# Kernel optimization log

Measured on AMD Instinct MI355X. Metric: run time of the kernel, lower is better.

The kernel has to match this reference:

```python
import jax, jax.numpy as jnp
import numpy as np

N_NODES = 100000
IN_CH = 128
HIDDEN = 256
N_EDGES = 500000


def setup_inputs() -> dict:
    key = jax.random.key(0)
    k1, k2, k3, k4, k5, k6 = jax.random.split(key, 6)
    latent_space = jax.random.normal(k1, (N_NODES, IN_CH), dtype=jnp.float32)
    edge_index = jax.random.randint(k2, (2, N_EDGES), 0, N_NODES, dtype=jnp.int64)
    # torch Linear params: W is [out, in], y = x @ W.T + b
    lim1 = 1.0 / np.sqrt(2 * IN_CH)
    W1 = jax.random.uniform(k3, (HIDDEN, 2 * IN_CH), minval=-lim1, maxval=lim1, dtype=jnp.float32)
    b1 = jax.random.uniform(k4, (HIDDEN,), minval=-lim1, maxval=lim1, dtype=jnp.float32)
    lim2 = 1.0 / np.sqrt(HIDDEN)
    W2 = jax.random.uniform(k5, (1, HIDDEN), minval=-lim2, maxval=lim2, dtype=jnp.float32)
    b2 = jax.random.uniform(k6, (1,), minval=-lim2, maxval=lim2, dtype=jnp.float32)
    return {"latent_space": latent_space, "W1": W1, "b1": b1, "W2": W2, "b2": b2,
            "edge_index": edge_index}


def reference(latent_space, W1, b1, W2, b2, edge_index):
    src, dst = edge_index[0], edge_index[1]
    h_src = latent_space[src]                      # [E, C]
    h_dst = latent_space[dst]                      # [E, C]
    h_pair = jnp.concatenate([h_src, h_dst], axis=1)  # [E, 2C]
    h = jax.nn.relu(h_pair @ W1.T + b1)            # [E, H]; dropout=0 (eval)
    logits = (h @ W2.T + b2).squeeze(-1)           # [E]
    return jax.nn.sigmoid(logits)
```

## Files before the change

### kernel.cpp

```cpp
#include <hip/hip_runtime.h>
#include <hip/hip_bf16.h>
#include <stdint.h>

#define M_NODES 100000
#define E_EDGES 500000
#define NCOL    512
#define HID     256

typedef unsigned short u16;
typedef u16   u16x8 __attribute__((ext_vector_type(8)));
typedef u16   u16x4 __attribute__((ext_vector_type(4)));
typedef __bf16 bf16x8 __attribute__((ext_vector_type(8)));
typedef float f32x4 __attribute__((ext_vector_type(4)));

static __device__ __forceinline__ u16 f2bf(float f) {
  uint32_t u = __float_as_uint(f);
  u += 0x7fff + ((u >> 16) & 1);
  return (u16)(u >> 16);
}
static __device__ __forceinline__ float bf2f(u16 h) {
  return __uint_as_float(((uint32_t)h) << 16);
}

__global__ __launch_bounds__(256) void k_convert(const float* __restrict__ in,
                                                 u16* __restrict__ out, int n4) {
  int i = blockIdx.x * blockDim.x + threadIdx.x;
  int stride = gridDim.x * blockDim.x;
  for (; i < n4; i += stride) {
    float4 f = reinterpret_cast<const float4*>(in)[i];
    u16x4 o;
    o[0] = f2bf(f.x); o[1] = f2bf(f.y); o[2] = f2bf(f.z); o[3] = f2bf(f.w);
    reinterpret_cast<u16x4*>(out)[i] = o;
  }
}

__global__ __launch_bounds__(256) void k_weights(const float* __restrict__ W1,
                                                 u16* __restrict__ Bt) {
  int idx = blockIdx.x * 256 + threadIdx.x;
  int j = idx >> 7, k = idx & 127;
  float w = (j < HID) ? W1[j * 256 + k] : W1[(j - HID) * 256 + 128 + k];
  Bt[idx] = f2bf(w);
}

__global__ __launch_bounds__(256, 2) void k_gemm(const u16* __restrict__ A,
                                                 const u16* __restrict__ Bt,
                                                 const float* __restrict__ b1,
                                                 u16* __restrict__ UV) {
  __shared__ __align__(16) u16 ldsA[128 * 128];
  __shared__ __align__(16) u16 ldsB[128 * 128];
  const int t = threadIdx.x;
  const int bm = blockIdx.x, bn = blockIdx.y;

  {
    const int sub = t >> 4;
    const int slot = t & 15;
    #pragma unroll
    for (int r = 0; r < 8; ++r) {
      int row = r * 16 + sub;
      int sw = (slot ^ (row & 7)) * 8;
      int grow = bm * 128 + row; if (grow > M_NODES - 1) grow = M_NODES - 1;
      u16x8 va = *reinterpret_cast<const u16x8*>(A + (size_t)grow * 128 + slot * 8);
      *reinterpret_cast<u16x8*>(&ldsA[row * 128 + sw]) = va;
      int brow = bn * 128 + row;
      u16x8 vb = *reinterpret_cast<const u16x8*>(Bt + (size_t)brow * 128 + slot * 8);
      *reinterpret_cast<u16x8*>(&ldsB[row * 128 + sw]) = vb;
    }
  }
  __syncthreads();

  const int w  = t >> 6;
  const int l  = t & 63;
  const int wm = (w >> 1) * 64;
  const int wn = (w & 1) * 64;
  const int lr = l & 15;
  const int lk = l >> 4;

  f32x4 acc[4][4];
  #pragma unroll
  for (int i = 0; i < 4; ++i)
    #pragma unroll
    for (int j = 0; j < 4; ++j) acc[i][j] = f32x4{0.f, 0.f, 0.f, 0.f};

  #pragma unroll
  for (int kk = 0; kk < 128; kk += 32) {
    const int s = (kk >> 3) + lk;
    bf16x8 fa[4], fb[4];
    #pragma unroll
    for (int mt = 0; mt < 4; ++mt) {
      int row = wm + mt * 16 + lr;
      fa[mt] = *reinterpret_cast<const bf16x8*>(&ldsA[row * 128 + ((s ^ (row & 7)) * 8)]);
    }
    #pragma unroll
    for (int nt = 0; nt < 4; ++nt) {
      int row = wn + nt * 16 + lr;
      fb[nt] = *reinterpret_cast<const bf16x8*>(&ldsB[row * 128 + ((s ^ (row & 7)) * 8)]);
    }
    #pragma unroll
    for (int nt = 0; nt < 4; ++nt)
      #pragma unroll
      for (int mt = 0; mt < 4; ++mt)
        acc[nt][mt] = __builtin_amdgcn_mfma_f32_16x16x32_bf16(fb[nt], fa[mt], acc[nt][mt], 0, 0, 0);
  }

  #pragma unroll
  for (int nt = 0; nt < 4; ++nt) {
    #pragma unroll
    for (int mt = 0; mt < 4; ++mt) {
      int mg = bm * 128 + wm + mt * 16 + lr;
      int ng = bn * 128 + wn + nt * 16 + lk * 4;
      if (mg < M_NODES) {
        u16x4 o;
        #pragma unroll
        for (int r = 0; r < 4; ++r) {
          float v = acc[nt][mt][r];
          int col = ng + r;
          if (col < HID) v += b1[col];
          o[r] = f2bf(v);
        }
        *reinterpret_cast<u16x4*>(&UV[(size_t)mg * NCOL + ng]) = o;
      }
    }
  }
}

__global__ __launch_bounds__(256) void k_edge(const u16* __restrict__ UV,
                                              const int* __restrict__ src,
                                              const int* __restrict__ dst,
                                              const float* __restrict__ W2,
                                              const float* __restrict__ b2p,
                                              float* __restrict__ out) {
  const int t = threadIdx.x;
  const int hl = t & 31;
  const int hw = blockIdx.x * 8 + (t >> 5);
  const int nhw = gridDim.x * 8;

  float w2r[8];
  #pragma unroll
  for (int i = 0; i < 8; ++i) w2r[i] = W2[hl * 8 + i];
  const float b2 = *b2p;

  for (int e = hw; e < E_EDGES; e += nhw) {
    int s = src[e];
    int d = dst[e];
    u16x8 uu = *reinterpret_cast<const u16x8*>(UV + (size_t)s * NCOL + hl * 8);
    u16x8 vv = *reinterpret_cast<const u16x8*>(UV + (size_t)d * NCOL + HID + hl * 8);
    float a = 0.f;
    #pragma unroll
    for (int i = 0; i < 8; ++i) {
      float h = bf2f(uu[i]) + bf2f(vv[i]);
      h = fmaxf(h, 0.f);
      a = fmaf(h, w2r[i], a);
    }
    a += __shfl_xor(a, 16, 64);
    a += __shfl_xor(a, 8, 64);
    a += __shfl_xor(a, 4, 64);
    a += __shfl_xor(a, 2, 64);
    a += __shfl_xor(a, 1, 64);
    if (hl == 0) {
      out[e] = 1.0f / (1.0f + __expf(-(a + b2)));
    }
  }
}

extern "C" void kernel_launch(void* const* d_in, const int* in_sizes, int n_in,
                              void* d_out, int out_size, void* d_ws, size_t ws_size,
                              hipStream_t stream) {
  const float* latent = (const float*)d_in[0];
  const float* W1     = (const float*)d_in[1];
  const float* b1     = (const float*)d_in[2];
  const float* W2     = (const float*)d_in[3];
  const float* b2     = (const float*)d_in[4];
  const int*   eidx   = (const int*)d_in[5];

  char* ws = (char*)d_ws;
  u16* latent_bf = (u16*)ws;
  u16* Btw       = (u16*)(ws + 25600000);
  u16* UV        = (u16*)(ws + 25600000 + 131072);

  k_convert<<<2048, 256, 0, stream>>>(latent, latent_bf, (M_NODES * 128) / 4);
  k_weights<<<256, 256, 0, stream>>>(W1, Btw);
  dim3 gg((M_NODES + 127) / 128, NCOL / 128);
  k_gemm<<<gg, 256, 0, stream>>>(latent_bf, Btw, b1, UV);
  k_edge<<<1024, 256, 0, stream>>>(UV, eidx, eidx + E_EDGES, W2, b2, (float*)d_out);
}
```

Before: 236.3 us.

## Use direct global-to-LDS loads in GEMM and widen per-lane edge gathers

The GEMM tile load now uses global_load_lds to write A and pre-swizzled B straight into shared memory, bypassing registers. To make that work, the weight prep kernel now writes B already XOR-swizzled, and the A source address is permuted per lane. The edge kernel now handles four edges per wavefront with 16 lanes each, and each lane loads 32 bytes per side. It also gets a larger grid and an occupancy hint. This is meant to cut register staging in the GEMM and raise the number of gathers in flight in the edge pass, at the cost of more complex addressing.

```diff
diff --git a/kernel.cpp b/kernel.cpp
--- a/kernel.cpp
+++ b/kernel.cpp
@@ -21,6 +21,11 @@
 static __device__ __forceinline__ float bf2f(u16 h) {
   return __uint_as_float(((uint32_t)h) << 16);
 }
+
+#define GLOAD_LDS16(g, lds)                                                          \
+  __builtin_amdgcn_global_load_lds(                                                  \
+      (const __attribute__((address_space(1))) uint32_t*)(g),                        \
+      (__attribute__((address_space(3))) uint32_t*)(lds), 16, 0, 0)
 
 __global__ __launch_bounds__(256) void k_convert(const float* __restrict__ in,
                                                  u16* __restrict__ out, int n4) {
@@ -37,7 +42,10 @@
 __global__ __launch_bounds__(256) void k_weights(const float* __restrict__ W1,
                                                  u16* __restrict__ Bt) {
   int idx = blockIdx.x * 256 + threadIdx.x;
-  int j = idx >> 7, k = idx & 127;
+  int j = idx >> 7, kk = idx & 127;
+  int s = kk >> 3, i = kk & 7;
+  int ls = s ^ (j & 7);
+  int k = ls * 8 + i;
   float w = (j < HID) ? W1[j * 256 + k] : W1[(j - HID) * 256 + 128 + k];
   Bt[idx] = f2bf(w);
 }
@@ -50,26 +58,24 @@
   __shared__ __align__(16) u16 ldsB[128 * 128];
   const int t = threadIdx.x;
   const int bm = blockIdx.x, bn = blockIdx.y;
+  const int w = t >> 6, l = t & 63;
 
   {
-    const int sub = t >> 4;
-    const int slot = t & 15;
-    #pragma unroll
-    for (int r = 0; r < 8; ++r) {
-      int row = r * 16 + sub;
-      int sw = (slot ^ (row & 7)) * 8;
-      int grow = bm * 128 + row; if (grow > M_NODES - 1) grow = M_NODES - 1;
-      u16x8 va = *reinterpret_cast<const u16x8*>(A + (size_t)grow * 128 + slot * 8);
-      *reinterpret_cast<u16x8*>(&ldsA[row * 128 + sw]) = va;
-      int brow = bn * 128 + row;
-      u16x8 vb = *reinterpret_cast<const u16x8*>(Bt + (size_t)brow * 128 + slot * 8);
-      *reinterpret_cast<u16x8*>(&ldsB[row * 128 + sw]) = vb;
+    const int lr4 = l >> 4;
+    const int ls  = l & 15;
+    #pragma unroll
+    for (int c = 0; c < 8; ++c) {
+      const int chunk = w * 8 + c;
+      const int row   = chunk * 4 + lr4;
+      int grow = bm * 128 + row;
+      if (grow >= M_NODES) grow = M_NODES - 1;
+      const int gslot = ls ^ (row & 7);
+      GLOAD_LDS16(A + (size_t)grow * 128 + gslot * 8, &ldsA[chunk * 512]);
+      GLOAD_LDS16(Bt + (size_t)bn * 16384 + chunk * 512 + l * 8, &ldsB[chunk * 512]);
     }
   }
   __syncthreads();
 
-  const int w  = t >> 6;
-  const int l  = t & 63;
   const int wm = (w >> 1) * 64;
   const int wn = (w & 1) * 64;
   const int lr = l & 15;
@@ -123,41 +129,52 @@
   }
 }
 
-__global__ __launch_bounds__(256) void k_edge(const u16* __restrict__ UV,
-                                              const int* __restrict__ src,
-                                              const int* __restrict__ dst,
-                                              const float* __restrict__ W2,
-                                              const float* __restrict__ b2p,
-                                              float* __restrict__ out) {
+__global__ __launch_bounds__(256, 8) void k_edge(const u16* __restrict__ UV,
+                                                 const int* __restrict__ src,
+                                                 const int* __restrict__ dst,
+                                                 const float* __restrict__ W2,
+                                                 const float* __restrict__ b2p,
+                                                 float* __restrict__ out) {
   const int t = threadIdx.x;
-  const int hl = t & 31;
-  const int hw = blockIdx.x * 8 + (t >> 5);
-  const int nhw = gridDim.x * 8;
-
-  float w2r[8];
-  #pragma unroll
-  for (int i = 0; i < 8; ++i) w2r[i] = W2[hl * 8 + i];
+  const int l = t & 63;
+  const int sub = l & 15;
+  const int eg = l >> 4;
+  const int wid = blockIdx.x * 4 + (t >> 6);
+  const int nw = gridDim.x * 4;
+
+  float w2r[16];
+  #pragma unroll
+  for (int i = 0; i < 16; ++i) w2r[i] = W2[sub * 16 + i];
   const float b2 = *b2p;
 
-  for (int e = hw; e < E_EDGES; e += nhw) {
-    int s = src[e];
-    int d = dst[e];
-    u16x8 uu = *reinterpret_cast<const u16x8*>(UV + (size_t)s * NCOL + hl * 8);
-    u16x8 vv = *reinterpret_cast<const u16x8*>(UV + (size_t)d * NCOL + HID + hl * 8);
+  for (int e = wid * 4; e < E_EDGES; e += nw * 4) {
+    const int s = src[e + eg];
+    const int d = dst[e + eg];
+    const u16* pu = UV + (size_t)s * NCOL + sub * 16;
+    const u16* pv = UV + (size_t)d * NCOL + HID + sub * 16;
+    u16x8 ua = *reinterpret_cast<const u16x8*>(pu);
+    u16x8 ub = *reinterpret_cast<const u16x8*>(pu + 8);
+    u16x8 va = *reinterpret_cast<const u16x8*>(pv);
+    u16x8 vb = *reinterpret_cast<const u16x8*>(pv + 8);
     float a = 0.f;
     #pragma unroll
     for (int i = 0; i < 8; ++i) {
-      float h = bf2f(uu[i]) + bf2f(vv[i]);
+      float h = bf2f(ua[i]) + bf2f(va[i]);
       h = fmaxf(h, 0.f);
       a = fmaf(h, w2r[i], a);
     }
-    a += __shfl_xor(a, 16, 64);
+    #pragma unroll
+    for (int i = 0; i < 8; ++i) {
+      float h = bf2f(ub[i]) + bf2f(vb[i]);
+      h = fmaxf(h, 0.f);
+      a = fmaf(h, w2r[8 + i], a);
+    }
+    a += __shfl_xor(a, 1, 64);
+    a += __shfl_xor(a, 2, 64);
+    a += __shfl_xor(a, 4, 64);
     a += __shfl_xor(a, 8, 64);
-    a += __shfl_xor(a, 4, 64);
-    a += __shfl_xor(a, 2, 64);
-    a += __shfl_xor(a, 1, 64);
-    if (hl == 0) {
-      out[e] = 1.0f / (1.0f + __expf(-(a + b2)));
+    if (sub == 0) {
+      out[e + eg] = 1.0f / (1.0f + __expf(-(a + b2)));
     }
   }
 }
@@ -181,5 +198,5 @@
   k_weights<<<256, 256, 0, stream>>>(W1, Btw);
   dim3 gg((M_NODES + 127) / 128, NCOL / 128);
   k_gemm<<<gg, 256, 0, stream>>>(latent_bf, Btw, b1, UV);
-  k_edge<<<1024, 256, 0, stream>>>(UV, eidx, eidx + E_EDGES, W2, b2, (float*)d_out);
-}
+  k_edge<<<2048, 256, 0, stream>>>(UV, eidx, eidx + E_EDGES, W2, b2, (float*)d_out);
+}
```

After: 233.2 us. Within noise of the previous version (-1.3%).
